# Kernel optimization log

Hardware: AMD Instinct MI355X
Metric: run time of the kernel (lower is better)

## Reference

```python
import jax, jax.numpy as jnp
import numpy as np

B, S, D, NH, NKV, HD, FF = 2, 2048, 2048, 16, 8, 128, 8192
EPS = 1e-6
ROPE_THETA = 10000.0


def rmsnorm(x, w):
    return x * jax.lax.rsqrt(jnp.mean(x * x, axis=-1, keepdims=True) + EPS) * w


def rotate_half(x):
    h = x.shape[-1] // 2
    return jnp.concatenate([-x[..., h:], x[..., :h]], axis=-1)


def setup_inputs() -> dict:
    key = jax.random.key(0)
    ks = jax.random.split(key, 32)
    sc = 0.02
    inp = {}
    inp['x'] = jax.random.normal(ks[0], (B, S, D), dtype=jnp.float32)
    pos = jnp.arange(S, dtype=jnp.float32)
    inv = 1.0 / (ROPE_THETA ** (jnp.arange(0, HD, 2, dtype=jnp.float32) / HD))
    fr = jnp.outer(pos, inv)
    emb = jnp.concatenate([fr, fr], axis=-1)  # [S, HD]
    inp['cos'] = jnp.broadcast_to(jnp.cos(emb)[None], (B, S, HD)).astype(jnp.float32)
    inp['sin'] = jnp.broadcast_to(jnp.sin(emb)[None], (B, S, HD)).astype(jnp.float32)
    inp['vision_token_mask'] = jax.random.randint(ks[1], (B, S), 0, 2) > 0
    inp['attn_norm_w'] = jnp.ones((D,), jnp.float32)
    inp['ffn_norm_w'] = jnp.ones((D,), jnp.float32)
    shapes = {
        'wq': (D, NH * HD), 'wk': (D, NKV * HD), 'wv': (D, NKV * HD), 'wo': (NH * HD, D),
        'mm_wq': (D, NH * HD), 'mm_wk': (D, NKV * HD), 'mm_wv': (D, NKV * HD), 'mm_wo': (NH * HD, D),
        'gate_w': (D, FF), 'up_w': (D, FF), 'down_w': (FF, D),
        'mm_gate_w': (D, FF), 'mm_up_w': (D, FF), 'mm_down_w': (FF, D),
    }
    for i, (name, shp) in enumerate(shapes.items()):
        inp[name] = jax.random.normal(ks[2 + i], shp, dtype=jnp.float32) * sc
    for name in ['q_norm_w', 'k_norm_w', 'mm_q_norm_w', 'mm_k_norm_w']:
        inp[name] = jnp.ones((HD,), jnp.float32)
    return inp


def gpt_block(x, cos, sin, mask, attn_norm_w, ffn_norm_w,
              wq, wk, wv, wo, mm_wq, mm_wk, mm_wv, mm_wo,
              q_norm_w, k_norm_w, mm_q_norm_w, mm_k_norm_w,
              gate_w, up_w, down_w, mm_gate_w, mm_up_w, mm_down_w):
    m2 = mask[..., None]            # [B,S,1]
    m4 = mask[:, :, None, None]     # [B,S,1,1]
    h = rmsnorm(x, attn_norm_w)
    # dual-path QKV: text tokens use plain weights, vision tokens use mm_* weights
    q_t = rmsnorm((h @ wq).reshape(B, S, NH, HD), q_norm_w)
    q_v = rmsnorm((h @ mm_wq).reshape(B, S, NH, HD), mm_q_norm_w)
    q = jnp.where(m4, q_v, q_t)
    k_t = rmsnorm((h @ wk).reshape(B, S, NKV, HD), k_norm_w)
    k_v = rmsnorm((h @ mm_wk).reshape(B, S, NKV, HD), mm_k_norm_w)
    k = jnp.where(m4, k_v, k_t)
    v = jnp.where(m2, h @ mm_wv, h @ wv).reshape(B, S, NKV, HD)
    # RoPE (unsqueeze over head dim)
    cu = cos[:, :, None, :]
    su = sin[:, :, None, :]
    q = q * cu + rotate_half(q) * su
    k = k * cu + rotate_half(k) * su
    # GQA repeat + causal attention
    rep = NH // NKV
    k_r = jnp.repeat(k, rep, axis=2)
    v_r = jnp.repeat(v, rep, axis=2)
    scale = 1.0 / jnp.sqrt(jnp.float32(HD))
    scores = jnp.einsum('bqhd,bkhd->bhqk', q, k_r) * scale
    causal = jnp.tril(jnp.ones((S, S), bool))
    scores = jnp.where(causal, scores, jnp.float32(-1e30))
    p = jax.nn.softmax(scores, axis=-1)
    attn = jnp.einsum('bhqk,bkhd->bqhd', p, v_r).reshape(B, S, NH * HD)
    attn_out = jnp.where(m2, attn @ mm_wo, attn @ wo)
    h2 = x + attn_out
    # dual-path SwiGLU FFN
    g = rmsnorm(h2, ffn_norm_w)
    ff_t = (jax.nn.silu(g @ gate_w) * (g @ up_w)) @ down_w
    ff_v = (jax.nn.silu(g @ mm_gate_w) * (g @ mm_up_w)) @ mm_down_w
    return h2 + jnp.where(m2, ff_v, ff_t)


def reference(x, cos, sin, vision_token_mask, attn_norm_w, ffn_norm_w,
              wq, wk, wv, wo, mm_wq, mm_wk, mm_wv, mm_wo,
              q_norm_w, k_norm_w, mm_q_norm_w, mm_k_norm_w,
              gate_w, up_w, down_w, mm_gate_w, mm_up_w, mm_down_w):
    return gpt_block(x, cos, sin, vision_token_mask, attn_norm_w, ffn_norm_w,
                     wq, wk, wv, wo, mm_wq, mm_wk, mm_wv, mm_wo,
                     q_norm_w, k_norm_w, mm_q_norm_w, mm_k_norm_w,
                     gate_w, up_w, down_w, mm_gate_w, mm_up_w, mm_down_w)
```

## Files before the change

### kernel.cpp

```cpp
#include <hip/hip_runtime.h>

typedef unsigned short u16;
typedef __bf16 bf16x8 __attribute__((ext_vector_type(8)));
typedef float f32x4 __attribute__((ext_vector_type(4)));

__device__ __forceinline__ u16 f2bf(float f) {
    unsigned u = __builtin_bit_cast(unsigned, f);
    u += 0x7fffu + ((u >> 16) & 1u);
    return (u16)(u >> 16);
}
__device__ __forceinline__ float bf2f(u16 v) {
    unsigned u = ((unsigned)v) << 16;
    return __builtin_bit_cast(float, u);
}
__device__ __forceinline__ void glds16(const void* g, void* l) {
    __builtin_amdgcn_global_load_lds(
        (const __attribute__((address_space(1))) unsigned*)g,
        (__attribute__((address_space(3))) unsigned*)l, 16, 0, 0);
}

__device__ __forceinline__ void xcd_map(int bid, int nloc, int TM, int& tm, int& tn)
{
    const int xcd = bid & 7;
    int l = bid >> 3;
    const int per = nloc << 3;
    const int fullC = TM >> 3;
    const int lFull = fullC * per;
    int c, tn_l, tmIn;
    if (l < lFull) { c = l / per; int r = l - c * per; tn_l = r >> 3; tmIn = r & 7; }
    else { int r = l - lFull; int sc = TM - (fullC << 3); c = fullC; tn_l = r / sc; tmIn = r % sc; }
    tm = (c << 3) + tmIn;
    tn = xcd * nloc + tn_l;
}

__device__ __forceinline__ void swz_src(int r, int sp, int& rs, int& ks)
{
    int e = (((r & 1) << 2) | sp) ^ ((r >> 1) & 7);
    rs = (r & ~1) | (e >> 2);
    ks = e & 3;
}
__device__ __forceinline__ int swz_rd(int row, int lg)
{
    int s8 = (((row & 1) << 2) | lg) ^ ((row >> 1) & 7);
    return (row >> 1) * 128 + s8 * 16;
}

__global__ __launch_bounds__(1024) void build_perm(
    const int* __restrict__ mask, int* __restrict__ perm, int* __restrict__ counts)
{
    __shared__ int sc[1024];
    int t = threadIdx.x;
    int m[4], cnt = 0;
#pragma unroll
    for (int j = 0; j < 4; j++) {
        m[j] = mask[t * 4 + j] != 0;
        cnt += (m[j] == 0);
    }
    sc[t] = cnt;
    __syncthreads();
    for (int off = 1; off < 1024; off <<= 1) {
        int v = (t >= off) ? sc[t - off] : 0;
        __syncthreads();
        sc[t] += v;
        __syncthreads();
    }
    int totT = sc[1023];
    int exT = sc[t] - cnt;
    int exV = t * 4 - exT;
    int pT = exT, pV = totT + exV;
#pragma unroll
    for (int j = 0; j < 4; j++) {
        if (m[j] == 0) perm[pT++] = t * 4 + j;
        else           perm[pV++] = t * 4 + j;
    }
    if (t == 0) { counts[0] = totT; counts[1] = 4096 - totT; }
}

__global__ __launch_bounds__(256) void transpose_bf16(
    const float* __restrict__ W, u16* __restrict__ Wt, int Kd, int Nd)
{
    __shared__ float tile[64][65];
    int k0 = blockIdx.x * 64, n0 = blockIdx.y * 64;
    int t = threadIdx.x;
    int rr = t >> 4, cc = (t & 15) * 4;
#pragma unroll
    for (int i = 0; i < 4; i++) {
        float4 v = *(const float4*)&W[(long)(k0 + i * 16 + rr) * Nd + n0 + cc];
        tile[i * 16 + rr][cc]     = v.x;
        tile[i * 16 + rr][cc + 1] = v.y;
        tile[i * 16 + rr][cc + 2] = v.z;
        tile[i * 16 + rr][cc + 3] = v.w;
    }
    __syncthreads();
    int nn = t >> 3, k8 = (t & 7) * 8;
#pragma unroll
    for (int i = 0; i < 2; i++) {
        int n = i * 32 + nn;
        u16 pk[8];
#pragma unroll
        for (int j = 0; j < 8; j++) pk[j] = f2bf(tile[k8 + j][n]);
        *(uint4*)&Wt[(long)(n0 + n) * Kd + k0 + k8] = *(const uint4*)pk;
    }
}

__global__ __launch_bounds__(256) void rms_x(
    const float* __restrict__ x, const float* __restrict__ w, u16* __restrict__ out)
{
    long row = blockIdx.x;
    int t = threadIdx.x, wave = t >> 6, lane = t & 63;
    const float4* x4 = (const float4*)(x + row * 2048);
    float4 a = x4[2 * t], b = x4[2 * t + 1];
    float ss = a.x*a.x + a.y*a.y + a.z*a.z + a.w*a.w
             + b.x*b.x + b.y*b.y + b.z*b.z + b.w*b.w;
#pragma unroll
    for (int m = 1; m < 64; m <<= 1) ss += __shfl_xor(ss, m);
    __shared__ float red[4];
    if (lane == 0) red[wave] = ss;
    __syncthreads();
    float tot = red[0] + red[1] + red[2] + red[3];
    float inv = rsqrtf(tot * (1.0f / 2048.0f) + 1e-6f);
    const float4* w4 = (const float4*)w;
    float4 wa = w4[2 * t], wb = w4[2 * t + 1];
    u16* op = out + row * 2048 + t * 8;
    op[0] = f2bf(a.x * inv * wa.x); op[1] = f2bf(a.y * inv * wa.y);
    op[2] = f2bf(a.z * inv * wa.z); op[3] = f2bf(a.w * inv * wa.w);
    op[4] = f2bf(b.x * inv * wb.x); op[5] = f2bf(b.y * inv * wb.y);
    op[6] = f2bf(b.z * inv * wb.z); op[7] = f2bf(b.w * inv * wb.w);
}

template <int EPI, bool PG, bool PC>
__global__ __launch_bounds__(512, 4) void gemm32(
    const u16* __restrict__ A, const u16* __restrict__ Bt0, const u16* __restrict__ Bt1,
    void* __restrict__ Cv,
    const int* __restrict__ perm, const int* __restrict__ counts, int N, int K)
{
    extern __shared__ u16 lds[];
    int tm, tn;
    xcd_map(blockIdx.x, N >> 11, 33, tm, tn);
    const int nT = counts[0];
    const int tT = (nT + 127) >> 7, tV = (4096 - nT + 127) >> 7;
    if (tm >= tT + tV) return;
    const bool vis = tm >= tT;
    const u16* Bt = vis ? Bt1 : Bt0;
    const int rowbase = vis ? nT + (tm - tT) * 128 : tm * 128;
    const int rowlim = vis ? 4096 : nT;
    const int tid = threadIdx.x;
    const int wave = tid >> 6, lane = tid & 63;
    const int wrbase = (wave >> 2) * 64, wcbase = (wave & 3) * 64;
    const int lr = lane & 15, lg = lane >> 4;
    const int n0 = tn * 256;
    const int t4 = tid >> 2, sp = tid & 3;
    const char* aSrc;
    const char* bSrc[2];
    {
        int rs, ks; swz_src(t4, sp, rs, ks);
        int gr = rowbase + rs; gr = gr < 4095 ? gr : 4095;
        long ar = PG ? perm[gr] : gr;
        aSrc = (const char*)A + ar * (long)K * 2 + ks * 16;
    }
#pragma unroll
    for (int c = 0; c < 2; c++) {
        int r = c * 128 + t4;
        int rs, ks; swz_src(r, sp, rs, ks);
        bSrc[c] = (const char*)Bt + (long)(n0 + rs) * K * 2 + ks * 16;
    }
    auto stage = [&](int kt, int bu) {
        char* ab = (char*)lds + bu * 24576;
        long ko = (long)kt * 64;
        glds16(aSrc + ko, ab + tid * 16);
#pragma unroll
        for (int c = 0; c < 2; c++)
            glds16(bSrc[c] + ko, ab + 8192 + c * 8192 + tid * 16);
    };
    auto ldA = [&](int bu, int mi) -> bf16x8 {
        const char* ab = (const char*)lds + bu * 24576;
        int row = wrbase + mi * 16 + lr;
        return *(const bf16x8*)(ab + swz_rd(row, lg));
    };
    auto ldB = [&](int bu, int ni) -> bf16x8 {
        const char* bb = (const char*)lds + bu * 24576 + 8192;
        int row = wcbase + ni * 16 + lr;
        return *(const bf16x8*)(bb + swz_rd(row, lg));
    };

    f32x4 acc[4][4] = {};
    const int nkt = K >> 5;
    stage(0, 0);
    stage(1, 1);
    for (int kt = 0; kt < nkt; ++kt) {
        const int bu = kt % 3;
        if (kt == nkt - 1) asm volatile("s_waitcnt vmcnt(0)" ::: "memory");
        else               asm volatile("s_waitcnt vmcnt(3)" ::: "memory");
        __builtin_amdgcn_s_barrier();
        if (kt + 2 < nkt) stage(kt + 2, (kt + 2) % 3);
        bf16x8 af[4], bq[4];
#pragma unroll
        for (int i = 0; i < 4; i++) af[i] = ldA(bu, i);
#pragma unroll
        for (int j = 0; j < 4; j++) bq[j] = ldB(bu, j);
        __builtin_amdgcn_s_setprio(1);
#pragma unroll
        for (int i = 0; i < 4; i++)
#pragma unroll
            for (int j = 0; j < 4; j++)
                acc[i][j] = __builtin_amdgcn_mfma_f32_16x16x32_bf16(
                    af[i], bq[j], acc[i][j], 0, 0, 0);
        __builtin_amdgcn_s_setprio(0);
    }
#pragma unroll
    for (int mi = 0; mi < 4; mi++)
#pragma unroll
        for (int r = 0; r < 4; r++) {
            int gr = rowbase + wrbase + mi * 16 + lg * 4 + r;
            if (gr >= rowlim) continue;
            long crow = PC ? (long)perm[gr] : (long)gr;
#pragma unroll
            for (int ni = 0; ni < 4; ni++) {
                long col = n0 + wcbase + ni * 16 + lr;
                ((u16*)Cv)[crow * (long)N + col] = f2bf(acc[mi][ni][r]);
            }
        }
}

__global__ __launch_bounds__(512, 4) void gemm_gu(
    const u16* __restrict__ A,
    const u16* __restrict__ Bg0, const u16* __restrict__ Bg1,
    const u16* __restrict__ Bu0, const u16* __restrict__ Bu1,
    u16* __restrict__ C,
    const int* __restrict__ perm, const int* __restrict__ counts, int N, int K)
{
    extern __shared__ u16 lds[];
    int tm, tn;
    xcd_map(blockIdx.x, N >> 10, 33, tm, tn);
    const int nT = counts[0];
    const int tT = (nT + 127) >> 7, tV = (4096 - nT + 127) >> 7;
    if (tm >= tT + tV) return;
    const bool vis = tm >= tT;
    const u16* Bg = vis ? Bg1 : Bg0;
    const u16* Bu = vis ? Bu1 : Bu0;
    const int rowbase = vis ? nT + (tm - tT) * 128 : tm * 128;
    const int rowlim = vis ? 4096 : nT;
    const int tid = threadIdx.x;
    const int wave = tid >> 6, lane = tid & 63;
    const int wrbase = (wave >> 2) * 64, wcbase = (wave & 3) * 32;
    const int lr = lane & 15, lg = lane >> 4;
    const int n0 = tn * 128;
    const int t4 = tid >> 2, sp = tid & 3;
    const char *aSrc, *gSrc, *uSrc;
    {
        int rs, ks; swz_src(t4, sp, rs, ks);
        int gr = rowbase + rs; gr = gr < 4095 ? gr : 4095;
        long ar = (long)perm[gr];
        aSrc = (const char*)A + ar * (long)K * 2 + ks * 16;
        gSrc = (const char*)Bg + (long)(n0 + rs) * K * 2 + ks * 16;
        uSrc = (const char*)Bu + (long)(n0 + rs) * K * 2 + ks * 16;
    }
    auto stage = [&](int kt, int bu) {
        char* ab = (char*)lds + bu * 24576;
        long ko = (long)kt * 64;
        glds16(aSrc + ko, ab + tid * 16);
        glds16(gSrc + ko, ab + 8192 + tid * 16);
        glds16(uSrc + ko, ab + 16384 + tid * 16);
    };
    auto ldA = [&](int bu, int mi) -> bf16x8 {
        const char* ab = (const char*)lds + bu * 24576;
        int row = wrbase + mi * 16 + lr;
        return *(const bf16x8*)(ab + swz_rd(row, lg));
    };
    auto ldGU = [&](int bu, int sub, int ni) -> bf16x8 {
        const char* p = (const char*)lds + bu * 24576 + 8192 + sub * 8192;
        int row = wcbase + ni * 16 + lr;
        return *(const bf16x8*)(p + swz_rd(row, lg));
    };

    f32x4 accg[4][2] = {}, accu[4][2] = {};
    const int nkt = K >> 5;
    stage(0, 0);
    stage(1, 1);
    for (int kt = 0; kt < nkt; ++kt) {
        const int bu = kt % 3;
        if (kt == nkt - 1) asm volatile("s_waitcnt vmcnt(0)" ::: "memory");
        else               asm volatile("s_waitcnt vmcnt(3)" ::: "memory");
        __builtin_amdgcn_s_barrier();
        if (kt + 2 < nkt) stage(kt + 2, (kt + 2) % 3);
        bf16x8 af[4], bg[2], bv[2];
#pragma unroll
        for (int i = 0; i < 4; i++) af[i] = ldA(bu, i);
#pragma unroll
        for (int j = 0; j < 2; j++) {
            bg[j] = ldGU(bu, 0, j);
            bv[j] = ldGU(bu, 1, j);
        }
        __builtin_amdgcn_s_setprio(1);
#pragma unroll
        for (int i = 0; i < 4; i++)
#pragma unroll
            for (int j = 0; j < 2; j++) {
                accg[i][j] = __builtin_amdgcn_mfma_f32_16x16x32_bf16(
                    af[i], bg[j], accg[i][j], 0, 0, 0);
                accu[i][j] = __builtin_amdgcn_mfma_f32_16x16x32_bf16(
                    af[i], bv[j], accu[i][j], 0, 0, 0);
            }
        __builtin_amdgcn_s_setprio(0);
    }
#pragma unroll
    for (int mi = 0; mi < 4; mi++)
#pragma unroll
        for (int r = 0; r < 4; r++) {
            int gr = rowbase + wrbase + mi * 16 + lg * 4 + r;
            if (gr >= rowlim) continue;
#pragma unroll
            for (int ni = 0; ni < 2; ni++) {
                long col = n0 + wcbase + ni * 16 + lr;
                float g = accg[mi][ni][r], u = accu[mi][ni][r];
                C[(long)gr * N + col] = f2bf(g / (1.0f + __expf(-g)) * u);
            }
        }
}

template <int EPI, bool PG, bool PC>
__global__ __launch_bounds__(512, 4) void gemmsq(
    const u16* __restrict__ A, const u16* __restrict__ Bt0, const u16* __restrict__ Bt1,
    void* __restrict__ Cv, const float* __restrict__ resid,
    const int* __restrict__ perm, const int* __restrict__ counts, int N, int K)
{
    extern __shared__ u16 lds[];
    int tm, tn;
    xcd_map(blockIdx.x, N >> 10, 33, tm, tn);
    const int nT = counts[0];
    const int tT = (nT + 127) >> 7, tV = (4096 - nT + 127) >> 7;
    if (tm >= tT + tV) return;
    const bool vis = tm >= tT;
    const u16* Bt = vis ? Bt1 : Bt0;
    const int rowbase = vis ? nT + (tm - tT) * 128 : tm * 128;
    const int rowlim = vis ? 4096 : nT;
    const int tid = threadIdx.x;
    const int wave = tid >> 6, lane = tid & 63;
    const int wrbase = (wave >> 2) * 64, wcbase = (wave & 3) * 32;
    const int lr = lane & 15, lg = lane >> 4;
    const int n0 = tn * 128;
    const int t4 = tid >> 2, sp = tid & 3;
    const char *aSrc, *bSrc;
    {
        int rs, ks; swz_src(t4, sp, rs, ks);
        int gr = rowbase + rs; gr = gr < 4095 ? gr : 4095;
        long ar = PG ? (long)perm[gr] : (long)gr;
        aSrc = (const char*)A + ar * (long)K * 2 + ks * 16;
        bSrc = (const char*)Bt + (long)(n0 + rs) * K * 2 + ks * 16;
    }
    auto stage = [&](int kt, int bu) {
        char* ab = (char*)lds + bu * 16384;
        long ko = (long)kt * 64;
        glds16(aSrc + ko, ab + tid * 16);
        glds16(bSrc + ko, ab + 8192 + tid * 16);
    };
    auto ldA = [&](int bu, int mi) -> bf16x8 {
        const char* ab = (const char*)lds + bu * 16384;
        int row = wrbase + mi * 16 + lr;
        return *(const bf16x8*)(ab + swz_rd(row, lg));
    };
    auto ldB = [&](int bu, int ni) -> bf16x8 {
        const char* bb = (const char*)lds + bu * 16384 + 8192;
        int row = wcbase + ni * 16 + lr;
        return *(const bf16x8*)(bb + swz_rd(row, lg));
    };

    f32x4 acc[4][2] = {};
    const int nkt = K >> 5;
    stage(0, 0);
    for (int kt = 0; kt < nkt; ++kt) {
        const int bu = kt & 1;
        __syncthreads();
        if (kt + 1 < nkt) stage(kt + 1, bu ^ 1);
        bf16x8 af[4], bq[2];
#pragma unroll
        for (int i = 0; i < 4; i++) af[i] = ldA(bu, i);
#pragma unroll
        for (int j = 0; j < 2; j++) bq[j] = ldB(bu, j);
        __builtin_amdgcn_s_setprio(1);
#pragma unroll
        for (int i = 0; i < 4; i++)
#pragma unroll
            for (int j = 0; j < 2; j++)
                acc[i][j] = __builtin_amdgcn_mfma_f32_16x16x32_bf16(
                    af[i], bq[j], acc[i][j], 0, 0, 0);
        __builtin_amdgcn_s_setprio(0);
    }
#pragma unroll
    for (int mi = 0; mi < 4; mi++)
#pragma unroll
        for (int r = 0; r < 4; r++) {
            int gr = rowbase + wrbase + mi * 16 + lg * 4 + r;
            if (gr >= rowlim) continue;
            long crow = PC ? (long)perm[gr] : (long)gr;
#pragma unroll
            for (int ni = 0; ni < 2; ni++) {
                long col = n0 + wcbase + ni * 16 + lr;
                long idx = crow * (long)N + col;
                ((float*)Cv)[idx] = resid[idx] + acc[mi][ni][r];
            }
        }
}

__global__ __launch_bounds__(256) void qk_fuse(
    const u16* __restrict__ p, const int* __restrict__ mask,
    const float* __restrict__ cs, const float* __restrict__ sn,
    const float* __restrict__ nwt, const float* __restrict__ nwv,
    u16* __restrict__ out, int H, int stride)
{
    int wave = threadIdx.x >> 6, lane = threadIdx.x & 63;
    int gw = blockIdx.x * 4 + wave;
    int tok = gw / H, h = gw % H;
    int b = tok >> 11, s = tok & 2047;
    const u16* src = p + (long)tok * stride + h * 128;
    const float* w = mask[tok] ? nwv : nwt;
    int d = lane * 2;
    float yx = bf2f(src[d]), yy = bf2f(src[d + 1]);
    float ss = yx * yx + yy * yy;
#pragma unroll
    for (int m = 1; m < 64; m <<= 1) ss += __shfl_xor(ss, m);
    float inv = rsqrtf(ss * (1.0f / 128.0f) + 1e-6f);
    float y0 = yx * inv * w[d], y1 = yy * inv * w[d + 1];
    float o0 = __shfl_xor(y0, 32), o1 = __shfl_xor(y1, 32);
    float sgn = (lane < 32) ? -1.0f : 1.0f;
    const float* cp = cs + (long)tok * 128 + d;
    const float* spn = sn + (long)tok * 128 + d;
    float r0 = y0 * cp[0] + sgn * o0 * spn[0];
    float r1 = y1 * cp[1] + sgn * o1 * spn[1];
    u16* op = out + (((long)b * H + h) * 2048 + s) * 128 + d;
    op[0] = f2bf(r0); op[1] = f2bf(r1);
}

__global__ __launch_bounds__(256) void v_fuse(
    const u16* __restrict__ vsrc, u16* __restrict__ outv, int stride)
{
    __shared__ u16 tile[32][33];
    int s0 = blockIdx.x * 32, d0 = blockIdx.y * 32;
    int bkv = blockIdx.z, b = bkv >> 3, kv = bkv & 7;
    int tx = threadIdx.x, ty = threadIdx.y;
#pragma unroll
    for (int i = 0; i < 32; i += 8) {
        long tok = (long)b * 2048 + s0 + ty + i;
        tile[ty + i][tx] = vsrc[tok * stride + kv * 128 + d0 + tx];
    }
    __syncthreads();
#pragma unroll
    for (int i = 0; i < 32; i += 8)
        outv[(((long)b * 8 + kv) * 128 + d0 + ty + i) * 2048 + s0 + tx] =
            tile[tx][ty + i];
}

__global__ __launch_bounds__(256) void attn_fwd(
    const u16* __restrict__ q, const u16* __restrict__ k,
    const u16* __restrict__ v, u16* __restrict__ out)
{
    __shared__ u16 Ks[32 * 128];
    __shared__ u16 Vs[128 * 32];
    __shared__ u16 Ps[4][16][40];
    const int tid = threadIdx.x, wave = tid >> 6, lane = tid & 63;
    const int lr = lane & 15, lg = lane >> 4;
    const int b = blockIdx.z, h = blockIdx.y, q0 = blockIdx.x * 64;
    const int kvh = h >> 1;
    const u16* qp = q + (((long)b * 16 + h) * 2048 + q0 + wave * 16) * 128;
    bf16x8 qf[4];
#pragma unroll
    for (int f = 0; f < 4; f++)
        qf[f] = *(const bf16x8*)(qp + (long)lr * 128 + f * 32 + lg * 8);
    const char* kbase = (const char*)(k + ((long)b * 8 + kvh) * 2048 * 128);
    const char* vbase = (const char*)(v + ((long)b * 8 + kvh) * 128 * 2048);
    f32x4 o[8] = {};
    float lsum[4] = {};
    const float sc2 = 0.08838834764831845f * 1.44269504088896f;
    const float MB = 16.5f;
    const int ntiles = (q0 + 64) >> 5;
    for (int t = 0; t < ntiles; ++t) {
        int kv0 = t * 32;
        __syncthreads();
#pragma unroll
        for (int j = 0; j < 2; j++) {
            int L = (j * 4 + wave) * 1024 + lane * 16;
            {
                int row = L >> 8, cb = L & 255;
                glds16(kbase + (long)(kv0 + row) * 256 + (cb ^ ((row & 7) << 4)),
                       (char*)Ks + (j * 4 + wave) * 1024);
            }
            {
                int row = L >> 6, cb = L & 63;
                glds16(vbase + (long)row * 4096 + kv0 * 2 + (cb ^ ((row & 3) << 4)),
                       (char*)Vs + (j * 4 + wave) * 1024);
            }
        }
        __syncthreads();
        f32x4 s[2] = {};
#pragma unroll
        for (int sub = 0; sub < 2; ++sub)
#pragma unroll
            for (int f = 0; f < 4; ++f) {
                int row = sub * 16 + lr;
                int cb = (f * 64 + lg * 16) ^ ((row & 7) << 4);
                bf16x8 kf = *(const bf16x8*)((const char*)Ks + row * 256 + cb);
                s[sub] = __builtin_amdgcn_mfma_f32_16x16x32_bf16(qf[f], kf, s[sub], 0, 0, 0);
            }
#pragma unroll
        for (int r = 0; r < 4; r++) {
            int rowg = q0 + wave * 16 + lg * 4 + r;
            float s0 = s[0][r] * sc2 - MB; if (kv0 + lr > rowg)      s0 = -1e30f;
            float s1 = s[1][r] * sc2 - MB; if (kv0 + 16 + lr > rowg) s1 = -1e30f;
            float p0 = exp2f(s0), p1 = exp2f(s1);
            lsum[r] += p0 + p1;
            int prow = lg * 4 + r;
            Ps[wave][prow][lr] = f2bf(p0);
            Ps[wave][prow][16 + lr] = f2bf(p1);
        }
        bf16x8 pf = *(const bf16x8*)&Ps[wave][lr][lg * 8];
#pragma unroll
        for (int ni = 0; ni < 8; ni++) {
            int row = ni * 16 + lr;
            int cb = (lg * 16) ^ ((row & 3) << 4);
            bf16x8 vf = *(const bf16x8*)((const char*)Vs + row * 64 + cb);
            o[ni] = __builtin_amdgcn_mfma_f32_16x16x32_bf16(pf, vf, o[ni], 0, 0, 0);
        }
    }
#pragma unroll
    for (int r = 0; r < 4; r++)
#pragma unroll
        for (int mm = 1; mm < 16; mm <<= 1) lsum[r] += __shfl_xor(lsum[r], mm);
#pragma unroll
    for (int ni = 0; ni < 8; ni++)
#pragma unroll
        for (int r = 0; r < 4; r++) {
            long row = (long)b * 2048 + q0 + wave * 16 + lg * 4 + r;
            out[row * 2048 + h * 128 + ni * 16 + lr] = f2bf(o[ni][r] / lsum[r]);
        }
}

extern "C" void kernel_launch(void* const* d_in, const int* in_sizes, int n_in,
                              void* d_out, int out_size, void* d_ws, size_t ws_size,
                              hipStream_t stream)
{
    const float* x    = (const float*)d_in[0];
    const float* cosp = (const float*)d_in[1];
    const float* sinp = (const float*)d_in[2];
    const int*   mask = (const int*)d_in[3];
    const float* anw  = (const float*)d_in[4];
    const float* fnw  = (const float*)d_in[5];
    const float* wq   = (const float*)d_in[6];
    const float* wk   = (const float*)d_in[7];
    const float* wv   = (const float*)d_in[8];
    const float* wo   = (const float*)d_in[9];
    const float* mwq  = (const float*)d_in[10];
    const float* mwk  = (const float*)d_in[11];
    const float* mwv  = (const float*)d_in[12];
    const float* mwo  = (const float*)d_in[13];
    const float* gw   = (const float*)d_in[14];
    const float* uw   = (const float*)d_in[15];
    const float* dw   = (const float*)d_in[16];
    const float* mgw  = (const float*)d_in[17];
    const float* muw  = (const float*)d_in[18];
    const float* mdw  = (const float*)d_in[19];
    const float* qnw  = (const float*)d_in[20];
    const float* knw  = (const float*)d_in[21];
    const float* mqnw = (const float*)d_in[22];
    const float* mknw = (const float*)d_in[23];

    char* base = (char*)d_ws;
    u16* wA0   = (u16*)(base);
    u16* wA1   = (u16*)(base + (32u << 20));
    u16* wB0   = (u16*)(base + (64u << 20));
    u16* wB1   = (u16*)(base + (96u << 20));
    u16* hbf   = (u16*)(base + (64u << 20));
    u16* qkv   = (u16*)(base + (80u << 20));
    u16* qb    = (u16*)(base + (112u << 20));
    u16* kb    = (u16*)(base + (128u << 20));
    u16* vb    = (u16*)(base + (136u << 20));
    u16* attnb = (u16*)(base + (144u << 20));
    u16* e1    = (u16*)(base + (128u << 20));
    float* h2  = (float*)(base + (192u << 20));
    u16* gbf   = (u16*)(base + (224u << 20));
    int* perm  = (int*)(base + (240u << 20));
    int* cnts  = perm + 4096;

    hipFuncSetAttribute((const void*)&gemm32<1, true, true>,
                        hipFuncAttributeMaxDynamicSharedMemorySize, 73728);
    hipFuncSetAttribute((const void*)&gemm_gu,
                        hipFuncAttributeMaxDynamicSharedMemorySize, 73728);

    auto TR = [&](const float* w, u16* dst, int K, int N) {
        transpose_bf16<<<dim3(K / 64, N / 64), 256, 0, stream>>>(w, dst, K, N);
    };

    build_perm<<<1, 1024, 0, stream>>>(mask, perm, cnts);
    rms_x<<<4096, 256, 0, stream>>>(x, anw, hbf);

    TR(wq, wA0, 2048, 2048);
    TR(wk, wA0 + (long)2048 * 2048, 2048, 1024);
    TR(wv, wA0 + (long)3072 * 2048, 2048, 1024);
    TR(mwq, wA1, 2048, 2048);
    TR(mwk, wA1 + (long)2048 * 2048, 2048, 1024);
    TR(mwv, wA1 + (long)3072 * 2048, 2048, 1024);
    gemm32<1, true, true><<<528, 512, 73728, stream>>>(
        hbf, wA0, wA1, (void*)qkv, perm, cnts, 4096, 2048);

    qk_fuse<<<16384, 256, 0, stream>>>(qkv, mask, cosp, sinp, qnw, mqnw, qb, 16, 4096);
    qk_fuse<<<8192, 256, 0, stream>>>(qkv + 2048, mask, cosp, sinp, knw, mknw, kb, 8, 4096);
    v_fuse<<<dim3(64, 4, 16), dim3(32, 8), 0, stream>>>(qkv + 3072, vb, 4096);

    attn_fwd<<<dim3(32, 16, 2), 256, 0, stream>>>(qb, kb, vb, attnb);

    TR(wo, wA0, 2048, 2048); TR(mwo, wA1, 2048, 2048);
    gemmsq<2, true, true><<<528, 512, 32768, stream>>>(
        attnb, wA0, wA1, (void*)h2, x, perm, cnts, 2048, 2048);

    rms_x<<<4096, 256, 0, stream>>>(h2, fnw, gbf);

    TR(gw, wA0, 2048, 8192); TR(mgw, wA1, 2048, 8192);
    TR(uw, wB0, 2048, 8192); TR(muw, wB1, 2048, 8192);
    gemm_gu<<<2112, 512, 73728, stream>>>(
        gbf, wA0, wA1, wB0, wB1, e1, perm, cnts, 8192, 2048);
    TR(dw, wA0, 8192, 2048); TR(mdw, wA1, 8192, 2048);
    gemmsq<2, false, true><<<528, 512, 32768, stream>>>(
        e1, wA0, wA1, (void*)d_out, h2, perm, cnts, 2048, 8192);
}
```

Measured before the change: 999.0 us.

## Use 64-wide KV tiles in attention and double-buffer gate/up GEMM

The attention kernel now processes 64 keys per iteration instead of 32. This halves the number of loop trips and block barriers, and each load phase brings in more K/V data. The gate/up GEMM goes from a three-stage to a two-stage LDS pipeline with __syncthreads, which cuts dynamic shared memory from 72KB to 48KB and may allow higher occupancy. The cost is less load latency hiding in the GEMM, plus the causal diagonal tile in attention now covers 64 keys.

New measurement: 1.033 ms. 3.4% more time.

```diff
diff --git a/kernel.cpp b/kernel.cpp
--- a/kernel.cpp
+++ b/kernel.cpp
@@ -276,13 +276,10 @@
     f32x4 accg[4][2] = {}, accu[4][2] = {};
     const int nkt = K >> 5;
     stage(0, 0);
-    stage(1, 1);
     for (int kt = 0; kt < nkt; ++kt) {
-        const int bu = kt % 3;
-        if (kt == nkt - 1) asm volatile("s_waitcnt vmcnt(0)" ::: "memory");
-        else               asm volatile("s_waitcnt vmcnt(3)" ::: "memory");
-        __builtin_amdgcn_s_barrier();
-        if (kt + 2 < nkt) stage(kt + 2, (kt + 2) % 3);
+        const int bu = kt & 1;
+        __syncthreads();
+        if (kt + 1 < nkt) stage(kt + 1, bu ^ 1);
         bf16x8 af[4], bg[2], bv[2];
 #pragma unroll
         for (int i = 0; i < 4; i++) af[i] = ldA(bu, i);
@@ -454,9 +451,9 @@
     const u16* __restrict__ q, const u16* __restrict__ k,
     const u16* __restrict__ v, u16* __restrict__ out)
 {
-    __shared__ u16 Ks[32 * 128];
-    __shared__ u16 Vs[128 * 32];
-    __shared__ u16 Ps[4][16][40];
+    __shared__ u16 Ks[64 * 128];
+    __shared__ u16 Vs[128 * 64];
+    __shared__ u16 Ps[4][16][72];
     const int tid = threadIdx.x, wave = tid >> 6, lane = tid & 63;
     const int lr = lane & 15, lg = lane >> 4;
     const int b = blockIdx.z, h = blockIdx.y, q0 = blockIdx.x * 64;
@@ -472,54 +469,63 @@
     float lsum[4] = {};
     const float sc2 = 0.08838834764831845f * 1.44269504088896f;
     const float MB = 16.5f;
-    const int ntiles = (q0 + 64) >> 5;
+    const int ntiles = (q0 >> 6) + 1;
     for (int t = 0; t < ntiles; ++t) {
-        int kv0 = t * 32;
+        long kv0 = (long)t * 64;
         __syncthreads();
 #pragma unroll
-        for (int j = 0; j < 2; j++) {
-            int L = (j * 4 + wave) * 1024 + lane * 16;
+        for (int c = 0; c < 4; c++) {
+            int L = c * 4096 + tid * 16;
             {
                 int row = L >> 8, cb = L & 255;
-                glds16(kbase + (long)(kv0 + row) * 256 + (cb ^ ((row & 7) << 4)),
-                       (char*)Ks + (j * 4 + wave) * 1024);
+                glds16(kbase + (kv0 + row) * 256 + (cb ^ ((row & 7) << 4)),
+                       (char*)Ks + L);
             }
             {
-                int row = L >> 6, cb = L & 63;
-                glds16(vbase + (long)row * 4096 + kv0 * 2 + (cb ^ ((row & 3) << 4)),
-                       (char*)Vs + (j * 4 + wave) * 1024);
+                int row = L >> 7, cb = L & 127;
+                glds16(vbase + (long)row * 4096 + kv0 * 2 + (cb ^ ((row & 7) << 4)),
+                       (char*)Vs + L);
             }
         }
         __syncthreads();
-        f32x4 s[2] = {};
-#pragma unroll
-        for (int sub = 0; sub < 2; ++sub)
+        f32x4 s[4] = {};
+#pragma unroll
+        for (int nf = 0; nf < 4; ++nf)
 #pragma unroll
             for (int f = 0; f < 4; ++f) {
-                int row = sub * 16 + lr;
+                int row = nf * 16 + lr;
                 int cb = (f * 64 + lg * 16) ^ ((row & 7) << 4);
                 bf16x8 kf = *(const bf16x8*)((const char*)Ks + row * 256 + cb);
-                s[sub] = __builtin_amdgcn_mfma_f32_16x16x32_bf16(qf[f], kf, s[sub], 0, 0, 0);
+                s[nf] = __builtin_amdgcn_mfma_f32_16x16x32_bf16(qf[f], kf, s[nf], 0, 0, 0);
             }
 #pragma unroll
         for (int r = 0; r < 4; r++) {
             int rowg = q0 + wave * 16 + lg * 4 + r;
-            float s0 = s[0][r] * sc2 - MB; if (kv0 + lr > rowg)      s0 = -1e30f;
-            float s1 = s[1][r] * sc2 - MB; if (kv0 + 16 + lr > rowg) s1 = -1e30f;
-            float p0 = exp2f(s0), p1 = exp2f(s1);
-            lsum[r] += p0 + p1;
-            int prow = lg * 4 + r;
-            Ps[wave][prow][lr] = f2bf(p0);
-            Ps[wave][prow][16 + lr] = f2bf(p1);
+            u16* prow = &Ps[wave][lg * 4 + r][0];
+            float ls = 0.0f;
+#pragma unroll
+            for (int nf = 0; nf < 4; nf++) {
+                float sv = s[nf][r] * sc2 - MB;
+                if (kv0 + nf * 16 + lr > rowg) sv = -1e30f;
+                float p = exp2f(sv);
+                ls += p;
+                prow[nf * 16 + lr] = f2bf(p);
+            }
+            lsum[r] += ls;
         }
-        bf16x8 pf = *(const bf16x8*)&Ps[wave][lr][lg * 8];
-#pragma unroll
-        for (int ni = 0; ni < 8; ni++) {
-            int row = ni * 16 + lr;
-            int cb = (lg * 16) ^ ((row & 3) << 4);
-            bf16x8 vf = *(const bf16x8*)((const char*)Vs + row * 64 + cb);
-            o[ni] = __builtin_amdgcn_mfma_f32_16x16x32_bf16(pf, vf, o[ni], 0, 0, 0);
-        }
+        bf16x8 pf[2];
+#pragma unroll
+        for (int kk = 0; kk < 2; kk++)
+            pf[kk] = *(const bf16x8*)&Ps[wave][lr][kk * 32 + lg * 8];
+#pragma unroll
+        for (int ni = 0; ni < 8; ni++)
+#pragma unroll
+            for (int kk = 0; kk < 2; kk++) {
+                int row = ni * 16 + lr;
+                int cb = (kk * 64 + lg * 16) ^ ((row & 7) << 4);
+                bf16x8 vf = *(const bf16x8*)((const char*)Vs + row * 128 + cb);
+                o[ni] = __builtin_amdgcn_mfma_f32_16x16x32_bf16(pf[kk], vf, o[ni], 0, 0, 0);
+            }
     }
 #pragma unroll
     for (int r = 0; r < 4; r++)
@@ -583,7 +589,7 @@
     hipFuncSetAttribute((const void*)&gemm32<1, true, true>,
                         hipFuncAttributeMaxDynamicSharedMemorySize, 73728);
     hipFuncSetAttribute((const void*)&gemm_gu,
-                        hipFuncAttributeMaxDynamicSharedMemorySize, 73728);
+                        hipFuncAttributeMaxDynamicSharedMemorySize, 49152);
 
     auto TR = [&](const float* w, u16* dst, int K, int N) {
         transpose_bf16<<<dim3(K / 64, N / 64), 256, 0, stream>>>(w, dst, K, N);
@@ -615,7 +621,7 @@
 
     TR(gw, wA0, 2048, 8192); TR(mgw, wA1, 2048, 8192);
     TR(uw, wB0, 2048, 8192); TR(muw, wB1, 2048, 8192);
-    gemm_gu<<<2112, 512, 73728, stream>>>(
+    gemm_gu<<<2112, 512, 49152, stream>>>(
         gbf, wA0, wA1, wB0, wB1, e1, perm, cnts, 8192, 2048);
     TR(dw, wA0, 8192, 2048); TR(mdw, wA1, 8192, 2048);
     gemmsq<2, false, true><<<528, 512, 32768, stream>>>(
```
